# Optimization experiments

Measured on AMD Instinct MI355X. Metric: run time of the kernel, lower is better.

## Reference

```python
import jax, jax.numpy as jnp
import numpy as np


def setup_inputs() -> dict:
    key = jax.random.key(0)
    k1, k2, k3 = jax.random.split(key, 3)
    B, M, N, D = 8, 12, 32, 256
    C = N * N          # Conv2d channel dim == N*N (see permute/view in source)
    R = 2              # reduction
    x = jax.random.normal(k1, (B, M, N, D), dtype=jnp.float32)
    W1 = jax.random.normal(k2, (C // R, C), dtype=jnp.float32) * 0.02  # Conv2d(C, C//R, 1, bias=False)
    W2 = jax.random.normal(k3, (C, C // R), dtype=jnp.float32) * 0.02  # Conv2d(C//R, C, 1, bias=False)
    return {"x": x, "W1": W1, "W2": W2}


def _mycorr(x):
    # Pearson correlation across feature dim D -> [B, M, N, N] adjacency
    xm = x - x.mean(axis=-1, keepdims=True)
    cov = jnp.einsum('bmnd,bmkd->bmnk', xm, xm)
    diag = jnp.diagonal(cov, axis1=-2, axis2=-1)                 # [B, M, N]
    norm = jnp.sqrt(jnp.clip(diag, 1e-12))
    return cov / (norm[..., :, None] * norm[..., None, :])


def reference(x, W1, W2):
    B, M, N, D = x.shape
    adj = _mycorr(x)

    # Fused pairwise-combo + mean over concat dim (2D):
    #   cat([Wh_i, pos_ij * Wh_j], -1).mean(-1) = (sum_d Wh_i + sum_d pos_ij*Wh_j) / (2D)
    # pos_ij[d] = 1 where Wh_i[d] == Wh_j[d] else 2   (source's where(diff==0, 1, 2))
    Wi = x[:, :, :, None, :]          # [B, M, N, 1, D]
    Wj = x[:, :, None, :, :]          # [B, M, 1, N, D]
    pos = jnp.where(Wi == Wj, jnp.float32(1.0), jnp.float32(2.0))
    e0 = (x.sum(-1)[:, :, :, None] + (pos * Wj).sum(-1)) / (2.0 * D)  # [B, M, N, N]

    # squeeze-excite style 1x1-conv MLP over the N*N channel dim
    ef = e0.reshape(B, M, N * N).transpose(0, 2, 1)                   # [B, C=N*N, M]
    h = jax.nn.relu(jnp.einsum('oc,bcm->bom', W1, ef))                # [B, C//R, M]
    e2 = jnp.einsum('co,bom->bcm', W2, h)                             # [B, C, M]
    e = jax.nn.sigmoid(e2.transpose(0, 2, 1).reshape(B, M, N, N))

    att = jnp.where(adj > 0, e, jnp.float32(-1e12))
    att = jax.nn.softmax(att, axis=-1)
    return jnp.einsum('bmnk,bmkd->bmnd', att, x)
```

## Files before the change

### kernel.cpp

```cpp
#include <hip/hip_runtime.h>


#define NGRP 12

__device__ unsigned int g_bar0[NGRP * 32];
__device__ unsigned int g_bar1[NGRP * 32];
__device__ unsigned int g_done[NGRP * 32];

__device__ __forceinline__ float dot4(float4 a, float4 b) {
    return a.x*b.x + a.y*b.y + a.z*b.z + a.w*b.w;
}
__device__ __forceinline__ void fma4(float4& acc, float s, float4 v) {
    acc.x += s*v.x; acc.y += s*v.y; acc.z += s*v.z; acc.w += s*v.w;
}

__device__ __forceinline__ void st_agent(float* p, float v) {
    __hip_atomic_store(p, v, __ATOMIC_RELAXED, __HIP_MEMORY_SCOPE_AGENT);
}
__device__ __forceinline__ float ld_agent(const float* p) {
    return __hip_atomic_load(p, __ATOMIC_RELAXED, __HIP_MEMORY_SCOPE_AGENT);
}
__device__ __forceinline__ unsigned long long ld_agent64(const unsigned long long* p) {
    return __hip_atomic_load(p, __ATOMIC_RELAXED, __HIP_MEMORY_SCOPE_AGENT);
}

__device__ __forceinline__ void bar_arrive(unsigned int* ctr) {
    __syncthreads();
    if (threadIdx.x == 0)
        __hip_atomic_fetch_add(ctr, 1u, __ATOMIC_RELAXED, __HIP_MEMORY_SCOPE_AGENT);
}
__device__ __forceinline__ void bar_wait(unsigned int* ctr) {
    if (threadIdx.x == 0) {
        while (__hip_atomic_load(ctr, __ATOMIC_RELAXED, __HIP_MEMORY_SCOPE_AGENT) < 16u)
            __builtin_amdgcn_s_sleep(2);
    }
    __syncthreads();
}

union RegionA {
    struct { float S[8][32]; float ef[8][1024]; } p1;
    struct { float4 xs4[32][65]; float S[32]; } p3;
};
union RegionB {
    float hl[8][512];
    float att[32][36];
};

__global__ __launch_bounds__(512) void fused(
        const float* __restrict__ x, const float* __restrict__ W1,
        const float* __restrict__ W2, float* __restrict__ out,
        float* __restrict__ Ht, float* __restrict__ Et)
{
    __shared__ RegionA A;
    __shared__ RegionB Bm;
    const int t = threadIdx.x;
    const int bid = blockIdx.x;
    const int g = bid >> 4;
    const int gi = g * 32;
    const float4* x4 = (const float4*)x;

    {
        const int oT = bid & 15;
        {
            const int n = t >> 4, dq = t & 15;
            #pragma unroll
            for (int bl = 0; bl < 8; ++bl) {
                const float4* xb = x4 + (g*8 + bl)*2048;
                float s = 0.f;
                #pragma unroll
                for (int j = 0; j < 4; ++j) {
                    float4 v = xb[n*64 + dq + 16*j];
                    s += v.x + v.y + v.z + v.w;
                }
                s += __shfl_xor(s, 1, 16);
                s += __shfl_xor(s, 2, 16);
                s += __shfl_xor(s, 4, 16);
                s += __shfl_xor(s, 8, 16);
                if (dq == 0) A.p1.S[bl][n] = s;
            }
        }
        __syncthreads();
        #pragma unroll
        for (int i = 0; i < 16; ++i) {
            int idx = t + 512*i;
            int bl = idx >> 10, c = idx & 1023;
            int nn = c >> 5, kk = c & 31;
            float sn = A.p1.S[bl][nn], sk = A.p1.S[bl][kk];
            A.p1.ef[bl][c] = (sn + 2.f*sk - (nn == kk ? sk : 0.f)) * (1.f/512.f);
        }
        __syncthreads();
        const int clane = t & 31, og = t >> 5;
        const int o0 = oT*32 + og;
        const float4* w40 = (const float4*)(W1 + o0*1024);
        const float4* w41 = (const float4*)(W1 + (o0+16)*1024);
        float acc0[8] = {0.f,0.f,0.f,0.f,0.f,0.f,0.f,0.f};
        float acc1[8] = {0.f,0.f,0.f,0.f,0.f,0.f,0.f,0.f};
        #pragma unroll
        for (int co = 0; co < 8; ++co) {
            float4 e[8];
            #pragma unroll
            for (int bl = 0; bl < 8; ++bl)
                e[bl] = *((const float4*)&A.p1.ef[bl][(co*32 + clane)*4]);
            float4 wa = w40[co*32 + clane];
            float4 wb = w41[co*32 + clane];
            #pragma unroll
            for (int bl = 0; bl < 8; ++bl) {
                acc0[bl] += dot4(wa, e[bl]);
                acc1[bl] += dot4(wb, e[bl]);
            }
        }
        #pragma unroll
        for (int bl = 0; bl < 8; ++bl) {
            float a = acc0[bl], b = acc1[bl];
            #pragma unroll
            for (int m = 1; m < 32; m <<= 1) {
                a += __shfl_xor(a, m, 32);
                b += __shfl_xor(b, m, 32);
            }
            acc0[bl] = a; acc1[bl] = b;
        }
        if (clane == 0) {
            #pragma unroll
            for (int bl = 0; bl < 8; ++bl) {
                int row = (g*8 + bl)*512;
                st_agent(&Ht[row + o0],      fmaxf(acc0[bl], 0.f));
                st_agent(&Ht[row + o0 + 16], fmaxf(acc1[bl], 0.f));
            }
        }
    }
    bar_arrive(&g_bar0[gi]);

    const int bm = bid >> 1, hh = bid & 1;
    {
        #pragma unroll
        for (int i = 0; i < 4; ++i) {
            int idx = t + 512*i;
            A.p3.xs4[idx >> 6][idx & 63] = x4[bm*2048 + idx];
        }
        __syncthreads();
        int r = t >> 4, dq = t & 15;
        float s = 0.f;
        #pragma unroll
        for (int j = 0; j < 4; ++j) {
            float4 v = A.p3.xs4[r][dq + 16*j];
            s += v.x + v.y + v.z + v.w;
        }
        s += __shfl_xor(s, 1, 16);
        s += __shfl_xor(s, 2, 16);
        s += __shfl_xor(s, 4, 16);
        s += __shfl_xor(s, 8, 16);
        if (dq == 0) A.p3.S[r] = s;
    }
    bar_wait(&g_bar0[gi]);

    {
        const int cQ = bid & 15;
        const unsigned long long* Ht8 =
            (const unsigned long long*)(Ht + (g*8)*512);
        #pragma unroll
        for (int j = 0; j < 4; ++j) {
            int pos = t + 512*j;
            unsigned long long v = ld_agent64(Ht8 + pos);
            int bl = pos >> 8, o2 = pos & 255;
            float2 f;
            f.x = __uint_as_float((unsigned)(v & 0xffffffffu));
            f.y = __uint_as_float((unsigned)(v >> 32));
            *((float2*)&Bm.hl[bl][o2*2]) = f;
        }
        __syncthreads();
        const int olane = t & 31, cgp = t >> 5;
        const int c0 = cQ*64 + cgp;
        const float4* w4a = (const float4*)(W2 + (c0     )*512);
        const float4* w4b = (const float4*)(W2 + (c0 + 16)*512);
        const float4* w4c = (const float4*)(W2 + (c0 + 32)*512);
        const float4* w4d = (const float4*)(W2 + (c0 + 48)*512);
        float accA[8] = {0.f,0.f,0.f,0.f,0.f,0.f,0.f,0.f};
        float accB[8] = {0.f,0.f,0.f,0.f,0.f,0.f,0.f,0.f};
        float accC[8] = {0.f,0.f,0.f,0.f,0.f,0.f,0.f,0.f};
        float accD[8] = {0.f,0.f,0.f,0.f,0.f,0.f,0.f,0.f};
        #pragma unroll
        for (int oo = 0; oo < 4; ++oo) {
            float4 hv[8];
            #pragma unroll
            for (int bl = 0; bl < 8; ++bl)
                hv[bl] = *((const float4*)&Bm.hl[bl][(oo*32 + olane)*4]);
            float4 wa = w4a[oo*32 + olane];
            float4 wb = w4b[oo*32 + olane];
            float4 wc = w4c[oo*32 + olane];
            float4 wd = w4d[oo*32 + olane];
            #pragma unroll
            for (int bl = 0; bl < 8; ++bl) {
                accA[bl] += dot4(wa, hv[bl]);
                accB[bl] += dot4(wb, hv[bl]);
                accC[bl] += dot4(wc, hv[bl]);
                accD[bl] += dot4(wd, hv[bl]);
            }
        }
        #pragma unroll
        for (int bl = 0; bl < 8; ++bl) {
            float a = accA[bl], b = accB[bl], c = accC[bl], d = accD[bl];
            #pragma unroll
            for (int m = 1; m < 32; m <<= 1) {
                a += __shfl_xor(a, m, 32);
                b += __shfl_xor(b, m, 32);
                c += __shfl_xor(c, m, 32);
                d += __shfl_xor(d, m, 32);
            }
            accA[bl]=a; accB[bl]=b; accC[bl]=c; accD[bl]=d;
        }
        if (olane == 0) {
            #pragma unroll
            for (int bl = 0; bl < 8; ++bl) {
                int row = (g*8 + bl)*1024;
                st_agent(&Et[row + c0],      1.f/(1.f + __expf(-accA[bl])));
                st_agent(&Et[row + c0 + 16], 1.f/(1.f + __expf(-accB[bl])));
                st_agent(&Et[row + c0 + 32], 1.f/(1.f + __expf(-accC[bl])));
                st_agent(&Et[row + c0 + 48], 1.f/(1.f + __expf(-accD[bl])));
            }
        }
    }
    bar_arrive(&g_bar1[gi]);

    const int gp = t >> 1, qh = t & 1;
    const int ga = gp >> 4, gb = gp & 15;
    float g00=0.f, g01=0.f, g10=0.f, g11=0.f;
    {
        const int qbase = qh * 32;
        #pragma unroll 8
        for (int qq = 0; qq < 32; ++qq) {
            int q = qbase + qq;
            float4 a0 = A.p3.xs4[ga][q],    a1 = A.p3.xs4[ga+16][q];
            float4 b0 = A.p3.xs4[gb][q],    b1 = A.p3.xs4[gb+16][q];
            g00 += dot4(a0,b0); g01 += dot4(a0,b1);
            g10 += dot4(a1,b0); g11 += dot4(a1,b1);
        }
        g00 += __shfl_xor(g00, 1, 2);
        g01 += __shfl_xor(g01, 1, 2);
        g10 += __shfl_xor(g10, 1, 2);
        g11 += __shfl_xor(g11, 1, 2);
    }
    float sa0 = A.p3.S[ga]    * (1.f/256.f);
    float sa1 = A.p3.S[ga+16] * (1.f/256.f);
    float sb0 = A.p3.S[gb], sb1 = A.p3.S[gb+16];
    bar_wait(&g_bar1[gi]);

    if (qh == 0) {
        const float* Eb = Et + bm*1024;
        float e00 = ld_agent(&Eb[ga*32 + gb]);
        float e01 = ld_agent(&Eb[ga*32 + gb+16]);
        float e10 = ld_agent(&Eb[(ga+16)*32 + gb]);
        float e11 = ld_agent(&Eb[(ga+16)*32 + gb+16]);
        Bm.att[ga][gb]       = (g00 - sa0*sb0) > 0.f ? e00 : -1e12f;
        Bm.att[ga][gb+16]    = (g01 - sa0*sb1) > 0.f ? e01 : -1e12f;
        Bm.att[ga+16][gb]    = (g10 - sa1*sb0) > 0.f ? e10 : -1e12f;
        Bm.att[ga+16][gb+16] = (g11 - sa1*sb1) > 0.f ? e11 : -1e12f;
    }
    __syncthreads();
    {
        int r = t >> 4, q = t & 15;
        float2 lg = *((const float2*)&Bm.att[r][q*2]);
        float m = fmaxf(lg.x, lg.y);
        m = fmaxf(m, __shfl_xor(m,1,16));
        m = fmaxf(m, __shfl_xor(m,2,16));
        m = fmaxf(m, __shfl_xor(m,4,16));
        m = fmaxf(m, __shfl_xor(m,8,16));
        float2 p;
        p.x = __expf(lg.x-m); p.y = __expf(lg.y-m);
        float s = p.x + p.y;
        s += __shfl_xor(s,1,16);
        s += __shfl_xor(s,2,16);
        s += __shfl_xor(s,4,16);
        s += __shfl_xor(s,8,16);
        float inv = 1.f/s;
        p.x*=inv; p.y*=inv;
        *((float2*)&Bm.att[r][q*2]) = p;
    }
    __syncthreads();
    {
        int txl = t & 31, wy = t >> 5;
        int r0 = wy*2;
        float4 acc0={0,0,0,0}, acc1={0,0,0,0};
        #pragma unroll
        for (int kq = 0; kq < 8; ++kq) {
            float4 xa = A.p3.xs4[kq*4+0][hh*32 + txl];
            float4 xb = A.p3.xs4[kq*4+1][hh*32 + txl];
            float4 xc = A.p3.xs4[kq*4+2][hh*32 + txl];
            float4 xd = A.p3.xs4[kq*4+3][hh*32 + txl];
            float4 w0 = *((const float4*)&Bm.att[r0+0][kq*4]);
            float4 w1 = *((const float4*)&Bm.att[r0+1][kq*4]);
            fma4(acc0,w0.x,xa); fma4(acc0,w0.y,xb); fma4(acc0,w0.z,xc); fma4(acc0,w0.w,xd);
            fma4(acc1,w1.x,xa); fma4(acc1,w1.y,xb); fma4(acc1,w1.z,xc); fma4(acc1,w1.w,xd);
        }
        float4* out4 = (float4*)out;
        int base = bm*2048 + hh*32 + txl;
        out4[base + (r0+0)*64] = acc0;
        out4[base + (r0+1)*64] = acc1;
    }

    if (t == 0) {
        unsigned int old = __hip_atomic_fetch_add(&g_done[gi], 1u,
                              __ATOMIC_RELAXED, __HIP_MEMORY_SCOPE_AGENT);
        if (old == 15u) {
            __hip_atomic_store(&g_bar0[gi], 0u, __ATOMIC_RELAXED, __HIP_MEMORY_SCOPE_AGENT);
            __hip_atomic_store(&g_bar1[gi], 0u, __ATOMIC_RELAXED, __HIP_MEMORY_SCOPE_AGENT);
            __hip_atomic_store(&g_done[gi], 0u, __ATOMIC_RELAXED, __HIP_MEMORY_SCOPE_AGENT);
        }
    }
}

extern "C" void kernel_launch(void* const* d_in, const int* in_sizes, int n_in,
                              void* d_out, int out_size, void* d_ws, size_t ws_size,
                              hipStream_t stream) {
    const float* x  = (const float*)d_in[0];
    const float* W1 = (const float*)d_in[1];
    const float* W2 = (const float*)d_in[2];
    float* out = (float*)d_out;
    float* ws  = (float*)d_ws;

    float* Ht = ws;
    float* Et = ws + 49152;

    fused<<<192, 512, 0, stream>>>(x, W1, W2, out, Ht, Et);
}
```

Measured before the change: 86.53 us.

## Fold e0 structure into W1 and split fused kernel into three launches

Because e0 depends only on the per-row sums of x, the first conv is rewritten as a product of a pre-reduced W1 (512x32) with the row sums. This replaces the 1024-wide contraction, and kA recomputes that reduced W1 on every call. The single persistent kernel with hand-rolled inter-block spin barriers is split into three ordinary kernels ordered by the stream, which removes the atomics and spin waits but adds launch gaps. kC also drops the split-q Gram reduction and uses only half the threads for the Gram step.

Result: slower. 88.53 us (+2.3%).

```diff
diff --git a/kernel.cpp b/kernel.cpp
--- a/kernel.cpp
+++ b/kernel.cpp
@@ -1,11 +1,5 @@
 #include <hip/hip_runtime.h>
 
-
-#define NGRP 12
-
-__device__ unsigned int g_bar0[NGRP * 32];
-__device__ unsigned int g_bar1[NGRP * 32];
-__device__ unsigned int g_done[NGRP * 32];
 
 __device__ __forceinline__ float dot4(float4 a, float4 b) {
     return a.x*b.x + a.y*b.y + a.z*b.z + a.w*b.w;
@@ -14,251 +8,183 @@
     acc.x += s*v.x; acc.y += s*v.y; acc.z += s*v.z; acc.w += s*v.w;
 }
 
-__device__ __forceinline__ void st_agent(float* p, float v) {
-    __hip_atomic_store(p, v, __ATOMIC_RELAXED, __HIP_MEMORY_SCOPE_AGENT);
-}
-__device__ __forceinline__ float ld_agent(const float* p) {
-    return __hip_atomic_load(p, __ATOMIC_RELAXED, __HIP_MEMORY_SCOPE_AGENT);
-}
-__device__ __forceinline__ unsigned long long ld_agent64(const unsigned long long* p) {
-    return __hip_atomic_load(p, __ATOMIC_RELAXED, __HIP_MEMORY_SCOPE_AGENT);
-}
-
-__device__ __forceinline__ void bar_arrive(unsigned int* ctr) {
-    __syncthreads();
-    if (threadIdx.x == 0)
-        __hip_atomic_fetch_add(ctr, 1u, __ATOMIC_RELAXED, __HIP_MEMORY_SCOPE_AGENT);
-}
-__device__ __forceinline__ void bar_wait(unsigned int* ctr) {
-    if (threadIdx.x == 0) {
-        while (__hip_atomic_load(ctr, __ATOMIC_RELAXED, __HIP_MEMORY_SCOPE_AGENT) < 16u)
-            __builtin_amdgcn_s_sleep(2);
-    }
-    __syncthreads();
-}
-
-union RegionA {
-    struct { float S[8][32]; float ef[8][1024]; } p1;
-    struct { float4 xs4[32][65]; float S[32]; } p3;
-};
-union RegionB {
-    float hl[8][512];
-    float att[32][36];
-};
-
-__global__ __launch_bounds__(512) void fused(
-        const float* __restrict__ x, const float* __restrict__ W1,
-        const float* __restrict__ W2, float* __restrict__ out,
-        float* __restrict__ Ht, float* __restrict__ Et)
-{
-    __shared__ RegionA A;
-    __shared__ RegionB Bm;
+__global__ __launch_bounds__(512) void kA(const float* __restrict__ x,
+                                          const float* __restrict__ W1,
+                                          float* __restrict__ W1A,
+                                          float* __restrict__ Ssum) {
+    __shared__ float w[16][1024];
+    const int t = threadIdx.x, bid = blockIdx.x;
+    if (bid < 32) {
+        const float4* W14 = (const float4*)(W1 + bid*16384);
+        float4* w4 = (float4*)&w[0][0];
+        #pragma unroll
+        for (int i = 0; i < 8; ++i) w4[t + 512*i] = W14[t + 512*i];
+        __syncthreads();
+        const int ol = t >> 5, n = t & 31;
+        const float* row = &w[ol][0];
+        float T1 = 0.f, T2 = 0.f;
+        #pragma unroll
+        for (int k = 0; k < 32; ++k) T1 += row[n*32 + ((k + n) & 31)];
+        #pragma unroll
+        for (int m = 0; m < 32; ++m) T2 += row[m*32 + n];
+        float diag = row[n*33];
+        W1A[(bid*16 + ol)*32 + n] = (T1 + 2.f*T2 - diag) * (1.f/512.f);
+    } else {
+        const int g = bid - 32;
+        const float4* x4 = (const float4*)x;
+        const int n = t >> 4, dq = t & 15;
+        #pragma unroll
+        for (int bl = 0; bl < 8; ++bl) {
+            const float4* xb = x4 + (g*8 + bl)*2048;
+            float s = 0.f;
+            #pragma unroll
+            for (int j = 0; j < 4; ++j) {
+                float4 v = xb[n*64 + dq + 16*j];
+                s += v.x + v.y + v.z + v.w;
+            }
+            s += __shfl_xor(s, 1, 16);
+            s += __shfl_xor(s, 2, 16);
+            s += __shfl_xor(s, 4, 16);
+            s += __shfl_xor(s, 8, 16);
+            if (dq == 0) Ssum[(g*8 + bl)*32 + n] = s;
+        }
+    }
+}
+
+__global__ __launch_bounds__(512) void kB(const float* __restrict__ W1A,
+                                          const float* __restrict__ Ssum,
+                                          const float* __restrict__ W2,
+                                          float* __restrict__ Et) {
+    __shared__ float S_l[8][32];
+    __shared__ float hl[8][512];
     const int t = threadIdx.x;
-    const int bid = blockIdx.x;
-    const int g = bid >> 4;
-    const int gi = g * 32;
+    const int cQ = blockIdx.x, g = blockIdx.y;
+    if (t < 256) ((float*)S_l)[t] = Ssum[g*256 + t];
+    __syncthreads();
+    {
+        const float4* wa = (const float4*)(W1A + t*32);
+        float4 w0=wa[0], w1=wa[1], w2=wa[2], w3=wa[3],
+               w4=wa[4], w5=wa[5], w6=wa[6], w7=wa[7];
+        #pragma unroll
+        for (int bl = 0; bl < 8; ++bl) {
+            const float4* s4 = (const float4*)&S_l[bl][0];
+            float a = dot4(w0,s4[0]) + dot4(w1,s4[1]) + dot4(w2,s4[2]) +
+                      dot4(w3,s4[3]) + dot4(w4,s4[4]) + dot4(w5,s4[5]) +
+                      dot4(w6,s4[6]) + dot4(w7,s4[7]);
+            hl[bl][t] = fmaxf(a, 0.f);
+        }
+    }
+    __syncthreads();
+    const int olane = t & 31, cgp = t >> 5;
+    const int c0 = cQ*64 + cgp;
+    const float4* w4a = (const float4*)(W2 + (c0     )*512);
+    const float4* w4b = (const float4*)(W2 + (c0 + 16)*512);
+    const float4* w4c = (const float4*)(W2 + (c0 + 32)*512);
+    const float4* w4d = (const float4*)(W2 + (c0 + 48)*512);
+    float accA[8] = {0.f,0.f,0.f,0.f,0.f,0.f,0.f,0.f};
+    float accB[8] = {0.f,0.f,0.f,0.f,0.f,0.f,0.f,0.f};
+    float accC[8] = {0.f,0.f,0.f,0.f,0.f,0.f,0.f,0.f};
+    float accD[8] = {0.f,0.f,0.f,0.f,0.f,0.f,0.f,0.f};
+    #pragma unroll
+    for (int oo = 0; oo < 4; ++oo) {
+        float4 hv[8];
+        #pragma unroll
+        for (int bl = 0; bl < 8; ++bl)
+            hv[bl] = *((const float4*)&hl[bl][(oo*32 + olane)*4]);
+        float4 wa = w4a[oo*32 + olane];
+        float4 wb = w4b[oo*32 + olane];
+        float4 wc = w4c[oo*32 + olane];
+        float4 wd = w4d[oo*32 + olane];
+        #pragma unroll
+        for (int bl = 0; bl < 8; ++bl) {
+            accA[bl] += dot4(wa, hv[bl]);
+            accB[bl] += dot4(wb, hv[bl]);
+            accC[bl] += dot4(wc, hv[bl]);
+            accD[bl] += dot4(wd, hv[bl]);
+        }
+    }
+    #pragma unroll
+    for (int bl = 0; bl < 8; ++bl) {
+        float a = accA[bl], b = accB[bl], c = accC[bl], d = accD[bl];
+        #pragma unroll
+        for (int m = 1; m < 32; m <<= 1) {
+            a += __shfl_xor(a, m, 32);
+            b += __shfl_xor(b, m, 32);
+            c += __shfl_xor(c, m, 32);
+            d += __shfl_xor(d, m, 32);
+        }
+        accA[bl]=a; accB[bl]=b; accC[bl]=c; accD[bl]=d;
+    }
+    if (olane == 0) {
+        #pragma unroll
+        for (int bl = 0; bl < 8; ++bl) {
+            int row = (g*8 + bl)*1024;
+            Et[row + c0]      = 1.f/(1.f + __expf(-accA[bl]));
+            Et[row + c0 + 16] = 1.f/(1.f + __expf(-accB[bl]));
+            Et[row + c0 + 32] = 1.f/(1.f + __expf(-accC[bl]));
+            Et[row + c0 + 48] = 1.f/(1.f + __expf(-accD[bl]));
+        }
+    }
+}
+
+__global__ __launch_bounds__(512) void kC(const float* __restrict__ x,
+                                          const float* __restrict__ Et,
+                                          float* __restrict__ out) {
+    __shared__ float4 xs4[32][65];
+    __shared__ float att[32][36];
+    __shared__ float S_l[32];
+    const int t = threadIdx.x;
+    const int bm = blockIdx.x >> 1, hh = blockIdx.x & 1;
     const float4* x4 = (const float4*)x;
 
-    {
-        const int oT = bid & 15;
-        {
-            const int n = t >> 4, dq = t & 15;
-            #pragma unroll
-            for (int bl = 0; bl < 8; ++bl) {
-                const float4* xb = x4 + (g*8 + bl)*2048;
-                float s = 0.f;
-                #pragma unroll
-                for (int j = 0; j < 4; ++j) {
-                    float4 v = xb[n*64 + dq + 16*j];
-                    s += v.x + v.y + v.z + v.w;
-                }
-                s += __shfl_xor(s, 1, 16);
-                s += __shfl_xor(s, 2, 16);
-                s += __shfl_xor(s, 4, 16);
-                s += __shfl_xor(s, 8, 16);
-                if (dq == 0) A.p1.S[bl][n] = s;
-            }
-        }
-        __syncthreads();
-        #pragma unroll
-        for (int i = 0; i < 16; ++i) {
-            int idx = t + 512*i;
-            int bl = idx >> 10, c = idx & 1023;
-            int nn = c >> 5, kk = c & 31;
-            float sn = A.p1.S[bl][nn], sk = A.p1.S[bl][kk];
-            A.p1.ef[bl][c] = (sn + 2.f*sk - (nn == kk ? sk : 0.f)) * (1.f/512.f);
-        }
-        __syncthreads();
-        const int clane = t & 31, og = t >> 5;
-        const int o0 = oT*32 + og;
-        const float4* w40 = (const float4*)(W1 + o0*1024);
-        const float4* w41 = (const float4*)(W1 + (o0+16)*1024);
-        float acc0[8] = {0.f,0.f,0.f,0.f,0.f,0.f,0.f,0.f};
-        float acc1[8] = {0.f,0.f,0.f,0.f,0.f,0.f,0.f,0.f};
-        #pragma unroll
-        for (int co = 0; co < 8; ++co) {
-            float4 e[8];
-            #pragma unroll
-            for (int bl = 0; bl < 8; ++bl)
-                e[bl] = *((const float4*)&A.p1.ef[bl][(co*32 + clane)*4]);
-            float4 wa = w40[co*32 + clane];
-            float4 wb = w41[co*32 + clane];
-            #pragma unroll
-            for (int bl = 0; bl < 8; ++bl) {
-                acc0[bl] += dot4(wa, e[bl]);
-                acc1[bl] += dot4(wb, e[bl]);
-            }
-        }
-        #pragma unroll
-        for (int bl = 0; bl < 8; ++bl) {
-            float a = acc0[bl], b = acc1[bl];
-            #pragma unroll
-            for (int m = 1; m < 32; m <<= 1) {
-                a += __shfl_xor(a, m, 32);
-                b += __shfl_xor(b, m, 32);
-            }
-            acc0[bl] = a; acc1[bl] = b;
-        }
-        if (clane == 0) {
-            #pragma unroll
-            for (int bl = 0; bl < 8; ++bl) {
-                int row = (g*8 + bl)*512;
-                st_agent(&Ht[row + o0],      fmaxf(acc0[bl], 0.f));
-                st_agent(&Ht[row + o0 + 16], fmaxf(acc1[bl], 0.f));
-            }
-        }
-    }
-    bar_arrive(&g_bar0[gi]);
-
-    const int bm = bid >> 1, hh = bid & 1;
-    {
-        #pragma unroll
-        for (int i = 0; i < 4; ++i) {
-            int idx = t + 512*i;
-            A.p3.xs4[idx >> 6][idx & 63] = x4[bm*2048 + idx];
-        }
-        __syncthreads();
+    #pragma unroll
+    for (int i = 0; i < 4; ++i) {
+        int idx = t + 512*i;
+        xs4[idx >> 6][idx & 63] = x4[bm*2048 + idx];
+    }
+    __syncthreads();
+    {
         int r = t >> 4, dq = t & 15;
         float s = 0.f;
         #pragma unroll
         for (int j = 0; j < 4; ++j) {
-            float4 v = A.p3.xs4[r][dq + 16*j];
+            float4 v = xs4[r][dq + 16*j];
             s += v.x + v.y + v.z + v.w;
         }
         s += __shfl_xor(s, 1, 16);
         s += __shfl_xor(s, 2, 16);
         s += __shfl_xor(s, 4, 16);
         s += __shfl_xor(s, 8, 16);
-        if (dq == 0) A.p3.S[r] = s;
-    }
-    bar_wait(&g_bar0[gi]);
-
-    {
-        const int cQ = bid & 15;
-        const unsigned long long* Ht8 =
-            (const unsigned long long*)(Ht + (g*8)*512);
-        #pragma unroll
-        for (int j = 0; j < 4; ++j) {
-            int pos = t + 512*j;
-            unsigned long long v = ld_agent64(Ht8 + pos);
-            int bl = pos >> 8, o2 = pos & 255;
-            float2 f;
-            f.x = __uint_as_float((unsigned)(v & 0xffffffffu));
-            f.y = __uint_as_float((unsigned)(v >> 32));
-            *((float2*)&Bm.hl[bl][o2*2]) = f;
-        }
-        __syncthreads();
-        const int olane = t & 31, cgp = t >> 5;
-        const int c0 = cQ*64 + cgp;
-        const float4* w4a = (const float4*)(W2 + (c0     )*512);
-        const float4* w4b = (const float4*)(W2 + (c0 + 16)*512);
-        const float4* w4c = (const float4*)(W2 + (c0 + 32)*512);
-        const float4* w4d = (const float4*)(W2 + (c0 + 48)*512);
-        float accA[8] = {0.f,0.f,0.f,0.f,0.f,0.f,0.f,0.f};
-        float accB[8] = {0.f,0.f,0.f,0.f,0.f,0.f,0.f,0.f};
-        float accC[8] = {0.f,0.f,0.f,0.f,0.f,0.f,0.f,0.f};
-        float accD[8] = {0.f,0.f,0.f,0.f,0.f,0.f,0.f,0.f};
-        #pragma unroll
-        for (int oo = 0; oo < 4; ++oo) {
-            float4 hv[8];
-            #pragma unroll
-            for (int bl = 0; bl < 8; ++bl)
-                hv[bl] = *((const float4*)&Bm.hl[bl][(oo*32 + olane)*4]);
-            float4 wa = w4a[oo*32 + olane];
-            float4 wb = w4b[oo*32 + olane];
-            float4 wc = w4c[oo*32 + olane];
-            float4 wd = w4d[oo*32 + olane];
-            #pragma unroll
-            for (int bl = 0; bl < 8; ++bl) {
-                accA[bl] += dot4(wa, hv[bl]);
-                accB[bl] += dot4(wb, hv[bl]);
-                accC[bl] += dot4(wc, hv[bl]);
-                accD[bl] += dot4(wd, hv[bl]);
-            }
-        }
-        #pragma unroll
-        for (int bl = 0; bl < 8; ++bl) {
-            float a = accA[bl], b = accB[bl], c = accC[bl], d = accD[bl];
-            #pragma unroll
-            for (int m = 1; m < 32; m <<= 1) {
-                a += __shfl_xor(a, m, 32);
-                b += __shfl_xor(b, m, 32);
-                c += __shfl_xor(c, m, 32);
-                d += __shfl_xor(d, m, 32);
-            }
-            accA[bl]=a; accB[bl]=b; accC[bl]=c; accD[bl]=d;
-        }
-        if (olane == 0) {
-            #pragma unroll
-            for (int bl = 0; bl < 8; ++bl) {
-                int row = (g*8 + bl)*1024;
-                st_agent(&Et[row + c0],      1.f/(1.f + __expf(-accA[bl])));
-                st_agent(&Et[row + c0 + 16], 1.f/(1.f + __expf(-accB[bl])));
-                st_agent(&Et[row + c0 + 32], 1.f/(1.f + __expf(-accC[bl])));
-                st_agent(&Et[row + c0 + 48], 1.f/(1.f + __expf(-accD[bl])));
-            }
-        }
-    }
-    bar_arrive(&g_bar1[gi]);
-
-    const int gp = t >> 1, qh = t & 1;
-    const int ga = gp >> 4, gb = gp & 15;
-    float g00=0.f, g01=0.f, g10=0.f, g11=0.f;
-    {
-        const int qbase = qh * 32;
+        if (dq == 0) S_l[r] = s;
+    }
+    __syncthreads();
+    if (t < 256) {
+        int a = t >> 4, b = t & 15;
+        float g00=0.f, g01=0.f, g10=0.f, g11=0.f;
         #pragma unroll 8
-        for (int qq = 0; qq < 32; ++qq) {
-            int q = qbase + qq;
-            float4 a0 = A.p3.xs4[ga][q],    a1 = A.p3.xs4[ga+16][q];
-            float4 b0 = A.p3.xs4[gb][q],    b1 = A.p3.xs4[gb+16][q];
+        for (int q = 0; q < 64; ++q) {
+            float4 a0 = xs4[a][q],    a1 = xs4[a+16][q];
+            float4 b0 = xs4[b][q],    b1 = xs4[b+16][q];
             g00 += dot4(a0,b0); g01 += dot4(a0,b1);
             g10 += dot4(a1,b0); g11 += dot4(a1,b1);
         }
-        g00 += __shfl_xor(g00, 1, 2);
-        g01 += __shfl_xor(g01, 1, 2);
-        g10 += __shfl_xor(g10, 1, 2);
-        g11 += __shfl_xor(g11, 1, 2);
-    }
-    float sa0 = A.p3.S[ga]    * (1.f/256.f);
-    float sa1 = A.p3.S[ga+16] * (1.f/256.f);
-    float sb0 = A.p3.S[gb], sb1 = A.p3.S[gb+16];
-    bar_wait(&g_bar1[gi]);
-
-    if (qh == 0) {
+        float sa0 = S_l[a]    * (1.f/256.f);
+        float sa1 = S_l[a+16] * (1.f/256.f);
+        float sb0 = S_l[b], sb1 = S_l[b+16];
         const float* Eb = Et + bm*1024;
-        float e00 = ld_agent(&Eb[ga*32 + gb]);
-        float e01 = ld_agent(&Eb[ga*32 + gb+16]);
-        float e10 = ld_agent(&Eb[(ga+16)*32 + gb]);
-        float e11 = ld_agent(&Eb[(ga+16)*32 + gb+16]);
-        Bm.att[ga][gb]       = (g00 - sa0*sb0) > 0.f ? e00 : -1e12f;
-        Bm.att[ga][gb+16]    = (g01 - sa0*sb1) > 0.f ? e01 : -1e12f;
-        Bm.att[ga+16][gb]    = (g10 - sa1*sb0) > 0.f ? e10 : -1e12f;
-        Bm.att[ga+16][gb+16] = (g11 - sa1*sb1) > 0.f ? e11 : -1e12f;
+        float e00 = Eb[a*32 + b];
+        float e01 = Eb[a*32 + b+16];
+        float e10 = Eb[(a+16)*32 + b];
+        float e11 = Eb[(a+16)*32 + b+16];
+        att[a][b]       = (g00 - sa0*sb0) > 0.f ? e00 : -1e12f;
+        att[a][b+16]    = (g01 - sa0*sb1) > 0.f ? e01 : -1e12f;
+        att[a+16][b]    = (g10 - sa1*sb0) > 0.f ? e10 : -1e12f;
+        att[a+16][b+16] = (g11 - sa1*sb1) > 0.f ? e11 : -1e12f;
     }
     __syncthreads();
     {
         int r = t >> 4, q = t & 15;
-        float2 lg = *((const float2*)&Bm.att[r][q*2]);
+        float2 lg = *((const float2*)&att[r][q*2]);
         float m = fmaxf(lg.x, lg.y);
         m = fmaxf(m, __shfl_xor(m,1,16));
         m = fmaxf(m, __shfl_xor(m,2,16));
@@ -273,7 +199,7 @@
         s += __shfl_xor(s,8,16);
         float inv = 1.f/s;
         p.x*=inv; p.y*=inv;
-        *((float2*)&Bm.att[r][q*2]) = p;
+        *((float2*)&att[r][q*2]) = p;
     }
     __syncthreads();
     {
@@ -282,12 +208,12 @@
         float4 acc0={0,0,0,0}, acc1={0,0,0,0};
         #pragma unroll
         for (int kq = 0; kq < 8; ++kq) {
-            float4 xa = A.p3.xs4[kq*4+0][hh*32 + txl];
-            float4 xb = A.p3.xs4[kq*4+1][hh*32 + txl];
-            float4 xc = A.p3.xs4[kq*4+2][hh*32 + txl];
-            float4 xd = A.p3.xs4[kq*4+3][hh*32 + txl];
-            float4 w0 = *((const float4*)&Bm.att[r0+0][kq*4]);
-            float4 w1 = *((const float4*)&Bm.att[r0+1][kq*4]);
+            float4 xa = xs4[kq*4+0][hh*32 + txl];
+            float4 xb = xs4[kq*4+1][hh*32 + txl];
+            float4 xc = xs4[kq*4+2][hh*32 + txl];
+            float4 xd = xs4[kq*4+3][hh*32 + txl];
+            float4 w0 = *((const float4*)&att[r0+0][kq*4]);
+            float4 w1 = *((const float4*)&att[r0+1][kq*4]);
             fma4(acc0,w0.x,xa); fma4(acc0,w0.y,xb); fma4(acc0,w0.z,xc); fma4(acc0,w0.w,xd);
             fma4(acc1,w1.x,xa); fma4(acc1,w1.y,xb); fma4(acc1,w1.z,xc); fma4(acc1,w1.w,xd);
         }
@@ -295,16 +221,6 @@
         int base = bm*2048 + hh*32 + txl;
         out4[base + (r0+0)*64] = acc0;
         out4[base + (r0+1)*64] = acc1;
-    }
-
-    if (t == 0) {
-        unsigned int old = __hip_atomic_fetch_add(&g_done[gi], 1u,
-                              __ATOMIC_RELAXED, __HIP_MEMORY_SCOPE_AGENT);
-        if (old == 15u) {
-            __hip_atomic_store(&g_bar0[gi], 0u, __ATOMIC_RELAXED, __HIP_MEMORY_SCOPE_AGENT);
-            __hip_atomic_store(&g_bar1[gi], 0u, __ATOMIC_RELAXED, __HIP_MEMORY_SCOPE_AGENT);
-            __hip_atomic_store(&g_done[gi], 0u, __ATOMIC_RELAXED, __HIP_MEMORY_SCOPE_AGENT);
-        }
     }
 }
 
@@ -317,8 +233,11 @@
     float* out = (float*)d_out;
     float* ws  = (float*)d_ws;
 
-    float* Ht = ws;
-    float* Et = ws + 49152;
-
-    fused<<<192, 512, 0, stream>>>(x, W1, W2, out, Ht, Et);
-}
+    float* W1A  = ws;
+    float* Ssum = ws + 16384;
+    float* Et   = ws + 19456;
+
+    kA<<<44, 512, 0, stream>>>(x, W1, W1A, Ssum);
+    kB<<<dim3(16, 12), 512, 0, stream>>>(W1A, Ssum, W2, Et);
+    kC<<<192, 512, 0, stream>>>(x, Et, out);
+}
```
